# Optimization experiments

Hardware: AMD Instinct MI355X
Metric: run time of the kernel (lower is better)

## Reference

```python
import jax, jax.numpy as jnp
import numpy as np

B, L, D, N = 8, 2048, 1024, 16


def setup_inputs() -> dict:
    key = jax.random.key(0)
    ks = jax.random.split(key, 7)
    x = jax.random.normal(ks[0], (B, L, D), dtype=jnp.float32)
    # A = -rand(d_model, d_state) - 0.5  -> in (-1.5, -0.5)
    A = -jax.random.uniform(ks[1], (D, N), dtype=jnp.float32) - 0.5
    # nn.Linear(d_model, d_state, bias=False): weight [N, D]
    Wb = jax.random.normal(ks[2], (N, D), dtype=jnp.float32) / np.sqrt(D)
    C = jax.random.normal(ks[3], (D, N), dtype=jnp.float32) * 0.1
    Dp = jax.random.normal(ks[4], (D,), dtype=jnp.float32) * 0.1
    # nn.Linear(d_model, d_model): weight [D, D], bias [D]
    Wd = jax.random.normal(ks[5], (D, D), dtype=jnp.float32) / np.sqrt(D)
    bd = jax.random.normal(ks[6], (D,), dtype=jnp.float32) * 0.01
    return {"x": x, "A": A, "Wb": Wb, "C": C, "Dp": Dp, "Wd": Wd, "bd": bd}


def reference(x, A, Wb, C, Dp, Wd, bd):
    # Precompute input-dependent projections for all timesteps (batched GEMMs)
    dt = jax.nn.softplus(jnp.einsum('bld,ed->ble', x, Wd) + bd)  # [B,L,D]
    Bx = jnp.einsum('bld,nd->bln', x, Wb)                        # [B,L,N]

    def step(h, inp):
        dt_t, bx_t, x_t = inp                  # [B,D], [B,N], [B,D]
        dA = dt_t[..., None] * A               # [B,D,N]
        h = jnp.exp(dA) * h + dt_t[..., None] * bx_t[:, None, :]
        y = jnp.einsum('bdn,dn->bd', h, C) + Dp * x_t
        return h, y

    h0 = jnp.zeros((x.shape[0], A.shape[0], A.shape[1]), dtype=x.dtype)
    xs = (jnp.swapaxes(dt, 0, 1), jnp.swapaxes(Bx, 0, 1), jnp.swapaxes(x, 0, 1))
    _, ys = jax.lax.scan(step, h0, xs)         # ys: [L,B,D]
    return jnp.swapaxes(ys, 0, 1)              # [B,L,D]
```

## Files before the change

kernel.cpp:

```cpp
#include <hip/hip_runtime.h>
#include <hip/hip_bf16.h>
#include <stdint.h>

#define B_ 8
#define L_ 2048
#define D_ 1024
#define N_ 16
#define M_ (B_ * L_)
#define K_ D_
#define SEG_ 64
#define SLEN_ (L_ / SEG_)
#define LOG2E 1.44269504088896341f

typedef __bf16 bf16;
typedef __bf16 bf16x8 __attribute__((ext_vector_type(8)));
typedef float f32x4 __attribute__((ext_vector_type(4)));

__global__ __launch_bounds__(256) void cvt_f32_bf16(const float* __restrict__ in,
                                                    bf16* __restrict__ out, int n4) {
  int i = blockIdx.x * 256 + threadIdx.x;
  const int stride = gridDim.x * 256;
  const float4* in4 = (const float4*)in;
  uint2* out2 = (uint2*)out;
  for (; i < n4; i += stride) {
    float4 v = in4[i];
    union { bf16 h[4]; uint2 u; } p;
    p.h[0] = (bf16)v.x; p.h[1] = (bf16)v.y; p.h[2] = (bf16)v.z; p.h[3] = (bf16)v.w;
    out2[i] = p.u;
  }
}

__device__ inline void gload_lds16(const bf16* g, bf16* l) {
  __builtin_amdgcn_global_load_lds(
      (const __attribute__((address_space(1))) void*)g,
      (__attribute__((address_space(3))) void*)l, 16, 0, 0);
}

__device__ inline float softplus_f(float z) {
  return fmaxf(z, 0.f) + __logf(1.f + __expf(-fabsf(z)));
}

__global__ __launch_bounds__(256) void gemm_dt(const bf16* __restrict__ Xb,
                                               const bf16* __restrict__ Wdb,
                                               const float* __restrict__ bd,
                                               bf16* __restrict__ dtb) {
  __shared__ bf16 As[2][128 * 32];
  __shared__ bf16 Bs[2][128 * 32];
  const int tid = threadIdx.x;
  const int lane = tid & 63;
  const int wave = tid >> 6;
  const int wr = wave >> 1, wc = wave & 1;
  const int virt = (blockIdx.x & 7) * 128 + (blockIdx.x >> 3);
  const int mt = virt >> 3, nt = virt & 7;
  const int m0 = mt * 128, n0 = nt * 128;

  const bf16* ga[2];
  const bf16* gb[2];
#pragma unroll
  for (int q = 0; q < 2; ++q) {
    const int c = tid + 256 * q;
    const int row = c >> 2;
    const int col8 = ((c & 3) ^ (row & 3)) * 8;
    ga[q] = Xb + (size_t)(m0 + row) * K_ + col8;
    gb[q] = Wdb + (size_t)(n0 + row) * K_ + col8;
  }

  f32x4 acc[4][4] = {};
  const int frow = (lane & 15);
  const int khalf = (lane >> 4);

  int aoff[4], boff[4];
#pragma unroll
  for (int i = 0; i < 4; ++i) {
    const int Ra = wr * 64 + i * 16 + frow;
    const int Rb = wc * 64 + i * 16 + frow;
    aoff[i] = Ra * 32 + (khalf ^ (Ra & 3)) * 8;
    boff[i] = Rb * 32 + (khalf ^ (Rb & 3)) * 8;
  }

#define STAGE_(buf, kt)                                         \
  {                                                             \
    gload_lds16(ga[0] + (kt), &As[buf][tid * 8]);               \
    gload_lds16(ga[1] + (kt), &As[buf][(tid + 256) * 8]);       \
    gload_lds16(gb[0] + (kt), &Bs[buf][tid * 8]);               \
    gload_lds16(gb[1] + (kt), &Bs[buf][(tid + 256) * 8]);       \
  }

  STAGE_(0, 0);
  __syncthreads();

  int cur = 0;
  for (int t = 0; t < K_ / 32; ++t) {
    if (t + 1 < K_ / 32) STAGE_(cur ^ 1, (t + 1) * 32);
    bf16x8 af[4], bfr[4];
#pragma unroll
    for (int i = 0; i < 4; ++i) af[i] = *(const bf16x8*)&As[cur][aoff[i]];
#pragma unroll
    for (int i = 0; i < 4; ++i) bfr[i] = *(const bf16x8*)&Bs[cur][boff[i]];
#pragma unroll
    for (int i = 0; i < 4; ++i)
#pragma unroll
      for (int j = 0; j < 4; ++j)
        acc[i][j] = __builtin_amdgcn_mfma_f32_16x16x32_bf16(af[i], bfr[j], acc[i][j], 0, 0, 0);
    __syncthreads();
    cur ^= 1;
  }
#undef STAGE_

  const int rbase = m0 + wr * 64 + (lane >> 4) * 4;
  const int cbase = n0 + wc * 64 + (lane & 15);
#pragma unroll
  for (int j = 0; j < 4; ++j) {
    const int col = cbase + j * 16;
    const float bias = bd[col];
#pragma unroll
    for (int i = 0; i < 4; ++i) {
      const int row = rbase + i * 16;
#pragma unroll
      for (int r = 0; r < 4; ++r) {
        float z = acc[i][j][r] + bias;
        dtb[(size_t)(row + r) * D_ + col] = (bf16)softplus_f(z);
      }
    }
  }
}

__global__ __launch_bounds__(256) void bx_mfma(const bf16* __restrict__ Xb,
                                               const bf16* __restrict__ Wbb,
                                               float* __restrict__ Bx) {
  const int lane = threadIdx.x & 63;
  const int wave = threadIdx.x >> 6;
  const int row0 = blockIdx.x * 64 + wave * 16;
  const int fr = lane & 15;
  const int kg = (lane >> 4) * 8;
  const bf16* ga = Xb + (size_t)(row0 + fr) * K_ + kg;
  const bf16* gb = Wbb + (size_t)fr * K_ + kg;
  f32x4 acc = {};
#pragma unroll 8
  for (int kt = 0; kt < K_; kt += 32) {
    bf16x8 af = *(const bf16x8*)(ga + kt);
    bf16x8 bf = *(const bf16x8*)(gb + kt);
    acc = __builtin_amdgcn_mfma_f32_16x16x32_bf16(af, bf, acc, 0, 0, 0);
  }
  const int orow = row0 + (lane >> 4) * 4;
  const int ocol = lane & 15;
#pragma unroll
  for (int r = 0; r < 4; ++r)
    Bx[(size_t)(orow + r) * N_ + ocol] = acc[r];
}

__global__ __launch_bounds__(256) void scan_p1(
    const bf16* __restrict__ dtb, const float* __restrict__ Bx,
    const float* __restrict__ A, bf16* __restrict__ hseg,
    float* __restrict__ stot) {
  const int tid = threadIdx.x;
  const int bi = blockIdx.x;
  const int seg = bi & 63;
  const int dtile = (bi >> 6) & 3;
  const int b = bi >> 8;
  const int d = dtile * 256 + tid;
  const int l0 = seg * SLEN_;

  const float* bxp = Bx + ((size_t)b * L_ + l0) * N_;

  float A2[N_];
  {
    const float4* ap = (const float4*)(A + (size_t)d * N_);
#pragma unroll
    for (int q = 0; q < 4; ++q) {
      float4 a = ap[q];
      A2[q * 4 + 0] = a.x * LOG2E; A2[q * 4 + 1] = a.y * LOG2E;
      A2[q * 4 + 2] = a.z * LOG2E; A2[q * 4 + 3] = a.w * LOG2E;
    }
  }

  const bf16* dtp = dtb + ((size_t)b * L_ + l0) * D_ + d;
  float h[N_] = {};
  float s = 0.f;

  float cdt[4];
#pragma unroll
  for (int u = 0; u < 4; ++u) cdt[u] = (float)dtp[(size_t)u * D_];

#define P1_STEP(i, c0)                                              \
  {                                                                 \
    s += (c0);                                                      \
    _Pragma("unroll")                                               \
    for (int q = 0; q < 4; ++q) {                                   \
      const float4 bv = *(const float4*)(bxp + (i) * N_ + q * 4);   \
      const float bvf[4] = {bv.x, bv.y, bv.z, bv.w};                \
      _Pragma("unroll")                                             \
      for (int j = 0; j < 4; ++j) {                                 \
        const int n = q * 4 + j;                                    \
        const float e = __builtin_amdgcn_exp2f((c0) * A2[n]);       \
        h[n] = fmaf(e, h[n], (c0) * bvf[j]);                        \
      }                                                             \
    }                                                               \
  }

  for (int i0 = 0; i0 < SLEN_ - 4; i0 += 4) {
#pragma unroll
    for (int u = 0; u < 4; ++u) {
      const int i = i0 + u;
      const float c0 = cdt[u];
      cdt[u] = (float)dtp[(size_t)(i + 4) * D_];
      P1_STEP(i, c0);
    }
  }
#pragma unroll
  for (int u = 0; u < 4; ++u) {
    const int i = SLEN_ - 4 + u;
    P1_STEP(i, cdt[u]);
  }
#undef P1_STEP

  bf16* hp = hseg + (((size_t)b * SEG_ + seg) * D_ + d) * N_;
  union { bf16 v[16]; uint4 u[2]; } pk;
#pragma unroll
  for (int n = 0; n < N_; ++n) pk.v[n] = (bf16)h[n];
  ((uint4*)hp)[0] = pk.u[0];
  ((uint4*)hp)[1] = pk.u[1];
  stot[((size_t)b * SEG_ + seg) * D_ + d] = s;
}

__global__ __launch_bounds__(256) void scan_combine(
    const float* __restrict__ A, bf16* __restrict__ hseg,
    const float* __restrict__ stot) {
  const int tid = threadIdx.x;
  const int bi = blockIdx.x;
  const int b = bi >> 6;
  const int d = (bi & 63) * 16 + (tid >> 4);
  const int n = tid & 15;
  const float A2 = A[(size_t)d * N_ + n] * LOG2E;

  const size_t hbase = ((size_t)b * SEG_ * D_ + d) * N_ + n;
  const size_t sbase = (size_t)b * SEG_ * D_ + d;
  float g = 0.f;
  float hs = (float)hseg[hbase];
  float st = stot[sbase];
  for (int sg = 0; sg < SEG_; ++sg) {
    const int s1 = (sg + 1 < SEG_) ? sg + 1 : sg;
    const float nhs = (float)hseg[hbase + (size_t)s1 * D_ * N_];
    const float nst = stot[sbase + (size_t)s1 * D_];
    hseg[hbase + (size_t)sg * D_ * N_] = (bf16)g;
    g = fmaf(__builtin_amdgcn_exp2f(A2 * st), g, hs);
    hs = nhs; st = nst;
  }
}

__global__ __launch_bounds__(256) void scan_p3(
    const bf16* __restrict__ dtb, const float* __restrict__ Bx,
    const bf16* __restrict__ xb, const float* __restrict__ A,
    const float* __restrict__ C, const float* __restrict__ Dp,
    const bf16* __restrict__ hseg, float* __restrict__ out) {
  const int tid = threadIdx.x;
  const int bi = blockIdx.x;
  const int seg = bi & 63;
  const int dtile = (bi >> 6) & 3;
  const int b = bi >> 8;
  const int d = dtile * 256 + tid;
  const int l0 = seg * SLEN_;

  const float* bxp = Bx + ((size_t)b * L_ + l0) * N_;

  float A2[N_], Cv[N_], h[N_];
  {
    const float4* ap = (const float4*)(A + (size_t)d * N_);
    const float4* cp = (const float4*)(C + (size_t)d * N_);
    const bf16* hp = hseg + (((size_t)b * SEG_ + seg) * D_ + d) * N_;
    union { uint4 u[2]; bf16 v[16]; } pk;
    pk.u[0] = ((const uint4*)hp)[0];
    pk.u[1] = ((const uint4*)hp)[1];
#pragma unroll
    for (int q = 0; q < 4; ++q) {
      float4 a = ap[q], c = cp[q];
      A2[q * 4 + 0] = a.x * LOG2E; A2[q * 4 + 1] = a.y * LOG2E;
      A2[q * 4 + 2] = a.z * LOG2E; A2[q * 4 + 3] = a.w * LOG2E;
      Cv[q * 4 + 0] = c.x; Cv[q * 4 + 1] = c.y;
      Cv[q * 4 + 2] = c.z; Cv[q * 4 + 3] = c.w;
    }
#pragma unroll
    for (int n = 0; n < N_; ++n) h[n] = (float)pk.v[n];
  }
  const float Dpv = Dp[d];

  const size_t base = ((size_t)b * L_ + l0) * D_ + d;
  const bf16* dtp = dtb + base;
  const bf16* xp = xb + base;
  float* op = out + base;

  float cdt[4], cx[4];
#pragma unroll
  for (int u = 0; u < 4; ++u) {
    cdt[u] = (float)dtp[(size_t)u * D_];
    cx[u]  = (float)xp[(size_t)u * D_];
  }

#define P3_STEP(i, c0, x0)                                          \
  {                                                                 \
    float y = Dpv * (x0);                                           \
    _Pragma("unroll")                                               \
    for (int q = 0; q < 4; ++q) {                                   \
      const float4 bv = *(const float4*)(bxp + (i) * N_ + q * 4);   \
      const float bvf[4] = {bv.x, bv.y, bv.z, bv.w};                \
      _Pragma("unroll")                                             \
      for (int j = 0; j < 4; ++j) {                                 \
        const int n = q * 4 + j;                                    \
        const float e = __builtin_amdgcn_exp2f((c0) * A2[n]);       \
        h[n] = fmaf(e, h[n], (c0) * bvf[j]);                        \
        y = fmaf(h[n], Cv[n], y);                                   \
      }                                                             \
    }                                                               \
    op[(size_t)(i) * D_] = y;                                       \
  }

  for (int i0 = 0; i0 < SLEN_ - 4; i0 += 4) {
#pragma unroll
    for (int u = 0; u < 4; ++u) {
      const int i = i0 + u;
      const float c0 = cdt[u], x0 = cx[u];
      cdt[u] = (float)dtp[(size_t)(i + 4) * D_];
      cx[u]  = (float)xp[(size_t)(i + 4) * D_];
      P3_STEP(i, c0, x0);
    }
  }
#pragma unroll
  for (int u = 0; u < 4; ++u) {
    const int i = SLEN_ - 4 + u;
    P3_STEP(i, cdt[u], cx[u]);
  }
#undef P3_STEP
}

extern "C" void kernel_launch(void* const* d_in, const int* in_sizes, int n_in,
                              void* d_out, int out_size, void* d_ws, size_t ws_size,
                              hipStream_t stream) {
  const float* x  = (const float*)d_in[0];
  const float* A  = (const float*)d_in[1];
  const float* Wb = (const float*)d_in[2];
  const float* C  = (const float*)d_in[3];
  const float* Dp = (const float*)d_in[4];
  const float* Wd = (const float*)d_in[5];
  const float* bd = (const float*)d_in[6];
  float* out = (float*)d_out;

  char* ws = (char*)d_ws;
  bf16*  dtb  = (bf16*)ws;
  bf16*  xb   = (bf16*)(ws + (size_t)33554432);
  bf16*  wdb  = (bf16*)(ws + (size_t)67108864);
  bf16*  wbb  = (bf16*)(ws + (size_t)69206016);
  float* bx   = (float*)(ws + (size_t)69238784);
  bf16*  hseg = (bf16*)(ws + (size_t)70287360);
  float* stot = (float*)(ws + (size_t)87064576);

  cvt_f32_bf16<<<2048, 256, 0, stream>>>(x, xb, M_ * K_ / 4);
  cvt_f32_bf16<<<1024, 256, 0, stream>>>(Wd, wdb, D_ * K_ / 4);
  cvt_f32_bf16<<<16, 256, 0, stream>>>(Wb, wbb, N_ * K_ / 4);
  bx_mfma<<<dim3(M_ / 64), 256, 0, stream>>>(xb, wbb, bx);
  gemm_dt<<<dim3((M_ / 128) * (D_ / 128)), 256, 0, stream>>>(xb, wdb, bd, dtb);
  scan_p1<<<dim3(B_ * 4 * SEG_), 256, 0, stream>>>(dtb, bx, A, hseg, stot);
  scan_combine<<<dim3(B_ * (D_ / 16)), 256, 0, stream>>>(A, hseg, stot);
  scan_p3<<<dim3(B_ * 4 * SEG_), 256, 0, stream>>>(dtb, bx, xb, A, C, Dp, hseg, out);
}
```

Baseline: 170.2 us.

## Fuse x conversion with Bx projection and pack scan math into float2

Merges the x fp32→bf16 conversion with the Bx MFMA projection, so x is read once and the bf16 copy is written while Bx is computed, with a split-K across waves reduced through shared memory. The two weight conversions become one launch. The scan kernels now keep their state in float2 vectors so the compiler can emit packed FP32 multiply/FMA instructions. This cuts launches and one full read of the bf16 x. The split-K adds an LDS reduction and a barrier, and the packed math changes the summation order of y slightly.

```diff
diff --git a/kernel.cpp b/kernel.cpp
--- a/kernel.cpp
+++ b/kernel.cpp
@@ -15,19 +15,66 @@
 typedef __bf16 bf16;
 typedef __bf16 bf16x8 __attribute__((ext_vector_type(8)));
 typedef float f32x4 __attribute__((ext_vector_type(4)));
-
-__global__ __launch_bounds__(256) void cvt_f32_bf16(const float* __restrict__ in,
-                                                    bf16* __restrict__ out, int n4) {
-  int i = blockIdx.x * 256 + threadIdx.x;
-  const int stride = gridDim.x * 256;
-  const float4* in4 = (const float4*)in;
-  uint2* out2 = (uint2*)out;
-  for (; i < n4; i += stride) {
-    float4 v = in4[i];
-    union { bf16 h[4]; uint2 u; } p;
-    p.h[0] = (bf16)v.x; p.h[1] = (bf16)v.y; p.h[2] = (bf16)v.z; p.h[3] = (bf16)v.w;
-    out2[i] = p.u;
-  }
+typedef float f32x2 __attribute__((ext_vector_type(2)));
+
+__global__ __launch_bounds__(256) void cvt_wdwb(const float* __restrict__ Wd,
+                                                const float* __restrict__ Wb,
+                                                bf16* __restrict__ wdb,
+                                                bf16* __restrict__ wbb) {
+  const int bi = blockIdx.x;
+  const float4* in4;
+  uint2* out2;
+  int i;
+  if (bi < 1024) {
+    i = bi * 256 + threadIdx.x;
+    in4 = (const float4*)Wd;
+    out2 = (uint2*)wdb;
+  } else {
+    i = (bi - 1024) * 256 + threadIdx.x;
+    in4 = (const float4*)Wb;
+    out2 = (uint2*)wbb;
+  }
+  float4 v = in4[i];
+  union { bf16 h[4]; uint2 u; } p;
+  p.h[0] = (bf16)v.x; p.h[1] = (bf16)v.y; p.h[2] = (bf16)v.z; p.h[3] = (bf16)v.w;
+  out2[i] = p.u;
+}
+
+__global__ __launch_bounds__(256) void prep_x(const float* __restrict__ x,
+                                              const bf16* __restrict__ Wbb,
+                                              bf16* __restrict__ xb,
+                                              float* __restrict__ Bx) {
+  const int lane = threadIdx.x & 63;
+  const int wave = threadIdx.x >> 6;
+  const int row0 = blockIdx.x * 16;
+  const int fr = lane & 15;
+  const int kg = (lane >> 4) * 8;
+  const int k0 = wave * 256;
+  const float* gx = x + (size_t)(row0 + fr) * K_ + k0 + kg;
+  const bf16* gb = Wbb + (size_t)fr * K_ + k0 + kg;
+  bf16* gxb = xb + (size_t)(row0 + fr) * K_ + k0 + kg;
+
+  f32x4 acc = {};
+#pragma unroll 8
+  for (int kt = 0; kt < 8; ++kt) {
+    float4 v0 = *(const float4*)(gx + kt * 32);
+    float4 v1 = *(const float4*)(gx + kt * 32 + 4);
+    union { bf16 h[8]; bf16x8 v; uint4 u; } p;
+    p.h[0] = (bf16)v0.x; p.h[1] = (bf16)v0.y; p.h[2] = (bf16)v0.z; p.h[3] = (bf16)v0.w;
+    p.h[4] = (bf16)v1.x; p.h[5] = (bf16)v1.y; p.h[6] = (bf16)v1.z; p.h[7] = (bf16)v1.w;
+    *(uint4*)(gxb + kt * 32) = p.u;
+    bf16x8 bf = *(const bf16x8*)(gb + kt * 32);
+    acc = __builtin_amdgcn_mfma_f32_16x16x32_bf16(p.v, bf, acc, 0, 0, 0);
+  }
+
+  __shared__ float red[4][16][17];
+  const int orow = (lane >> 4) * 4, ocol = fr;
+#pragma unroll
+  for (int r = 0; r < 4; ++r) red[wave][orow + r][ocol] = acc[r];
+  __syncthreads();
+  const int rr = threadIdx.x >> 4, cc = threadIdx.x & 15;
+  const float s = red[0][rr][cc] + red[1][rr][cc] + red[2][rr][cc] + red[3][rr][cc];
+  Bx[(size_t)(row0 + rr) * N_ + cc] = s;
 }
 
 __device__ inline void gload_lds16(const bf16* g, bf16* l) {
@@ -125,30 +172,6 @@
   }
 }
 
-__global__ __launch_bounds__(256) void bx_mfma(const bf16* __restrict__ Xb,
-                                               const bf16* __restrict__ Wbb,
-                                               float* __restrict__ Bx) {
-  const int lane = threadIdx.x & 63;
-  const int wave = threadIdx.x >> 6;
-  const int row0 = blockIdx.x * 64 + wave * 16;
-  const int fr = lane & 15;
-  const int kg = (lane >> 4) * 8;
-  const bf16* ga = Xb + (size_t)(row0 + fr) * K_ + kg;
-  const bf16* gb = Wbb + (size_t)fr * K_ + kg;
-  f32x4 acc = {};
-#pragma unroll 8
-  for (int kt = 0; kt < K_; kt += 32) {
-    bf16x8 af = *(const bf16x8*)(ga + kt);
-    bf16x8 bf = *(const bf16x8*)(gb + kt);
-    acc = __builtin_amdgcn_mfma_f32_16x16x32_bf16(af, bf, acc, 0, 0, 0);
-  }
-  const int orow = row0 + (lane >> 4) * 4;
-  const int ocol = lane & 15;
-#pragma unroll
-  for (int r = 0; r < 4; ++r)
-    Bx[(size_t)(orow + r) * N_ + ocol] = acc[r];
-}
-
 __global__ __launch_bounds__(256) void scan_p1(
     const bf16* __restrict__ dtb, const float* __restrict__ Bx,
     const float* __restrict__ A, bf16* __restrict__ hseg,
@@ -163,39 +186,40 @@
 
   const float* bxp = Bx + ((size_t)b * L_ + l0) * N_;
 
-  float A2[N_];
+  f32x2 A22[8];
   {
     const float4* ap = (const float4*)(A + (size_t)d * N_);
 #pragma unroll
     for (int q = 0; q < 4; ++q) {
       float4 a = ap[q];
-      A2[q * 4 + 0] = a.x * LOG2E; A2[q * 4 + 1] = a.y * LOG2E;
-      A2[q * 4 + 2] = a.z * LOG2E; A2[q * 4 + 3] = a.w * LOG2E;
+      A22[2 * q]     = (f32x2){a.x * LOG2E, a.y * LOG2E};
+      A22[2 * q + 1] = (f32x2){a.z * LOG2E, a.w * LOG2E};
     }
   }
 
   const bf16* dtp = dtb + ((size_t)b * L_ + l0) * D_ + d;
-  float h[N_] = {};
+  f32x2 h2[8] = {};
   float s = 0.f;
 
   float cdt[4];
 #pragma unroll
   for (int u = 0; u < 4; ++u) cdt[u] = (float)dtp[(size_t)u * D_];
 
-#define P1_STEP(i, c0)                                              \
-  {                                                                 \
-    s += (c0);                                                      \
-    _Pragma("unroll")                                               \
-    for (int q = 0; q < 4; ++q) {                                   \
-      const float4 bv = *(const float4*)(bxp + (i) * N_ + q * 4);   \
-      const float bvf[4] = {bv.x, bv.y, bv.z, bv.w};                \
-      _Pragma("unroll")                                             \
-      for (int j = 0; j < 4; ++j) {                                 \
-        const int n = q * 4 + j;                                    \
-        const float e = __builtin_amdgcn_exp2f((c0) * A2[n]);       \
-        h[n] = fmaf(e, h[n], (c0) * bvf[j]);                        \
-      }                                                             \
-    }                                                               \
+#define P1_STEP(i, c0)                                                   \
+  {                                                                      \
+    s += (c0);                                                           \
+    const f32x2 c2 = {(c0), (c0)};                                       \
+    _Pragma("unroll")                                                    \
+    for (int q = 0; q < 4; ++q) {                                        \
+      const float4 bv = *(const float4*)(bxp + (i) * N_ + q * 4);        \
+      const f32x2 b0 = {bv.x, bv.y}, b1 = {bv.z, bv.w};                  \
+      f32x2 g0 = c2 * A22[2 * q];                                        \
+      f32x2 g1 = c2 * A22[2 * q + 1];                                    \
+      f32x2 e0 = {__builtin_amdgcn_exp2f(g0.x), __builtin_amdgcn_exp2f(g0.y)}; \
+      f32x2 e1 = {__builtin_amdgcn_exp2f(g1.x), __builtin_amdgcn_exp2f(g1.y)}; \
+      h2[2 * q]     = e0 * h2[2 * q]     + c2 * b0;                      \
+      h2[2 * q + 1] = e1 * h2[2 * q + 1] + c2 * b1;                      \
+    }                                                                    \
   }
 
   for (int i0 = 0; i0 < SLEN_ - 4; i0 += 4) {
@@ -217,7 +241,10 @@
   bf16* hp = hseg + (((size_t)b * SEG_ + seg) * D_ + d) * N_;
   union { bf16 v[16]; uint4 u[2]; } pk;
 #pragma unroll
-  for (int n = 0; n < N_; ++n) pk.v[n] = (bf16)h[n];
+  for (int m = 0; m < 8; ++m) {
+    pk.v[2 * m] = (bf16)h2[m].x;
+    pk.v[2 * m + 1] = (bf16)h2[m].y;
+  }
   ((uint4*)hp)[0] = pk.u[0];
   ((uint4*)hp)[1] = pk.u[1];
   stot[((size_t)b * SEG_ + seg) * D_ + d] = s;
@@ -263,7 +290,7 @@
 
   const float* bxp = Bx + ((size_t)b * L_ + l0) * N_;
 
-  float A2[N_], Cv[N_], h[N_];
+  f32x2 A22[8], Cv2[8], h2[8];
   {
     const float4* ap = (const float4*)(A + (size_t)d * N_);
     const float4* cp = (const float4*)(C + (size_t)d * N_);
@@ -274,13 +301,14 @@
 #pragma unroll
     for (int q = 0; q < 4; ++q) {
       float4 a = ap[q], c = cp[q];
-      A2[q * 4 + 0] = a.x * LOG2E; A2[q * 4 + 1] = a.y * LOG2E;
-      A2[q * 4 + 2] = a.z * LOG2E; A2[q * 4 + 3] = a.w * LOG2E;
-      Cv[q * 4 + 0] = c.x; Cv[q * 4 + 1] = c.y;
-      Cv[q * 4 + 2] = c.z; Cv[q * 4 + 3] = c.w;
-    }
-#pragma unroll
-    for (int n = 0; n < N_; ++n) h[n] = (float)pk.v[n];
+      A22[2 * q]     = (f32x2){a.x * LOG2E, a.y * LOG2E};
+      A22[2 * q + 1] = (f32x2){a.z * LOG2E, a.w * LOG2E};
+      Cv2[2 * q]     = (f32x2){c.x, c.y};
+      Cv2[2 * q + 1] = (f32x2){c.z, c.w};
+    }
+#pragma unroll
+    for (int m = 0; m < 8; ++m)
+      h2[m] = (f32x2){(float)pk.v[2 * m], (float)pk.v[2 * m + 1]};
   }
   const float Dpv = Dp[d];
 
@@ -296,22 +324,24 @@
     cx[u]  = (float)xp[(size_t)u * D_];
   }
 
-#define P3_STEP(i, c0, x0)                                          \
-  {                                                                 \
-    float y = Dpv * (x0);                                           \
-    _Pragma("unroll")                                               \
-    for (int q = 0; q < 4; ++q) {                                   \
-      const float4 bv = *(const float4*)(bxp + (i) * N_ + q * 4);   \
-      const float bvf[4] = {bv.x, bv.y, bv.z, bv.w};                \
-      _Pragma("unroll")                                             \
-      for (int j = 0; j < 4; ++j) {                                 \
-        const int n = q * 4 + j;                                    \
-        const float e = __builtin_amdgcn_exp2f((c0) * A2[n]);       \
-        h[n] = fmaf(e, h[n], (c0) * bvf[j]);                        \
-        y = fmaf(h[n], Cv[n], y);                                   \
-      }                                                             \
-    }                                                               \
-    op[(size_t)(i) * D_] = y;                                       \
+#define P3_STEP(i, c0, x0)                                               \
+  {                                                                      \
+    const f32x2 c2 = {(c0), (c0)};                                       \
+    f32x2 y2 = {Dpv * (x0), 0.f};                                        \
+    _Pragma("unroll")                                                    \
+    for (int q = 0; q < 4; ++q) {                                        \
+      const float4 bv = *(const float4*)(bxp + (i) * N_ + q * 4);        \
+      const f32x2 b0 = {bv.x, bv.y}, b1 = {bv.z, bv.w};                  \
+      f32x2 g0 = c2 * A22[2 * q];                                        \
+      f32x2 g1 = c2 * A22[2 * q + 1];                                    \
+      f32x2 e0 = {__builtin_amdgcn_exp2f(g0.x), __builtin_amdgcn_exp2f(g0.y)}; \
+      f32x2 e1 = {__builtin_amdgcn_exp2f(g1.x), __builtin_amdgcn_exp2f(g1.y)}; \
+      h2[2 * q]     = e0 * h2[2 * q]     + c2 * b0;                      \
+      h2[2 * q + 1] = e1 * h2[2 * q + 1] + c2 * b1;                      \
+      y2 = y2 + h2[2 * q] * Cv2[2 * q];                                  \
+      y2 = y2 + h2[2 * q + 1] * Cv2[2 * q + 1];                          \
+    }                                                                    \
+    op[(size_t)(i) * D_] = y2.x + y2.y;                                  \
   }
 
   for (int i0 = 0; i0 < SLEN_ - 4; i0 += 4) {
@@ -353,10 +383,8 @@
   bf16*  hseg = (bf16*)(ws + (size_t)70287360);
   float* stot = (float*)(ws + (size_t)87064576);
 
-  cvt_f32_bf16<<<2048, 256, 0, stream>>>(x, xb, M_ * K_ / 4);
-  cvt_f32_bf16<<<1024, 256, 0, stream>>>(Wd, wdb, D_ * K_ / 4);
-  cvt_f32_bf16<<<16, 256, 0, stream>>>(Wb, wbb, N_ * K_ / 4);
-  bx_mfma<<<dim3(M_ / 64), 256, 0, stream>>>(xb, wbb, bx);
+  cvt_wdwb<<<1040, 256, 0, stream>>>(Wd, Wb, wdb, wbb);
+  prep_x<<<dim3(M_ / 16), 256, 0, stream>>>(x, wbb, xb, bx);
   gemm_dt<<<dim3((M_ / 128) * (D_ / 128)), 256, 0, stream>>>(xb, wdb, bd, dtb);
   scan_p1<<<dim3(B_ * 4 * SEG_), 256, 0, stream>>>(dtb, bx, A, hseg, stot);
   scan_combine<<<dim3(B_ * (D_ / 16)), 256, 0, stream>>>(A, hseg, stot);
```

Result: faster. 165.3 us (-2.9%).
